# Performance work log

Hardware: AMD Instinct MI355X
Metric: run time of the kernel (lower is better)

The kernel has to match this reference:

```python
import jax, jax.numpy as jnp
import numpy as np

NUM_HEADS = 12
EPS = 1e-6


def setup_inputs() -> dict:
    key = jax.random.key(0)
    k1, k2, k3, k4 = jax.random.split(key, 4)
    N, B, D = 1025, 8, 768
    x = jax.random.normal(k1, (N, B, D), dtype=jnp.float32)
    # torch nn.Linear weights: [out_features, in_features]
    w_qkv = jax.random.normal(k2, (3 * D, D), dtype=jnp.float32) * (D ** -0.5)
    w_proj = jax.random.normal(k3, (D, D), dtype=jnp.float32) * (D ** -0.5)
    b_proj = jax.random.normal(k4, (D,), dtype=jnp.float32) * 0.01
    return {"x": x, "w_qkv": w_qkv, "w_proj": w_proj, "b_proj": b_proj}


def reference(x, w_qkv, w_proj, b_proj):
    N, B, D = x.shape
    H = NUM_HEADS
    hd = D // H
    scale = hd ** -0.5
    scale_vv = scale * 1.0  # scale_multiplier = 1.0

    xb = jnp.transpose(x, (1, 0, 2))  # [B, N, D]
    qkv = xb @ w_qkv.T  # [B, N, 3D]
    qkv = qkv.reshape(B, N, 3, H, hd).transpose(2, 0, 3, 1, 4)  # [3, B, H, N, hd]
    q, k, v = qkv[0], qkv[1], qkv[2]

    # QK path: only row 0 of out_ori survives the masking, compute just that row
    scores0 = jnp.einsum('bhqd,bhkd->bhqk', q[:, :, :1], k) * scale  # [B,H,1,N]
    attn0 = jax.nn.softmax(scores0, axis=-1)
    out0 = jnp.einsum('bhqk,bhkd->bhqd', attn0, v)  # [B,H,1,hd]

    # VV cosine path: only rows 1: survive
    vn = v / jnp.maximum(jnp.linalg.norm(v, axis=-1, keepdims=True), EPS)
    scores_vv = jnp.einsum('bhqd,bhkd->bhqk', vn[:, :, 1:], vn) * scale_vv  # [B,H,N-1,N]
    attn_vv = jax.nn.softmax(scores_vv, axis=-1)
    out_vv = jnp.einsum('bhqk,bhkd->bhqd', attn_vv, v)  # [B,H,N-1,hd]

    out = jnp.concatenate([out0, out_vv], axis=2)  # [B,H,N,hd]
    out = out.transpose(0, 2, 1, 3).reshape(B, N, D)
    out = out @ w_proj.T + b_proj
    return jnp.transpose(out, (1, 0, 2))  # [N, B, D]
```

## Files before the change

kernel.cpp:

```cpp
#include <hip/hip_runtime.h>

typedef unsigned short u16;
typedef unsigned int   u32;
typedef __attribute__((ext_vector_type(8))) short short8;
typedef __attribute__((ext_vector_type(4))) float f32x4;

#define AS1 __attribute__((address_space(1)))
#define AS3 __attribute__((address_space(3)))

#define NSEQ  1025
#define BB    8
#define DD    768
#define HH    12
#define MROWS 8200
#define MPAD  8320
#define KPAD  1088

__device__ __forceinline__ void gl2lds16(const void* g, void* l) {
  __builtin_amdgcn_global_load_lds((const AS1 u32*)g, (AS3 u32*)l, 16, 0, 0);
}
__device__ __forceinline__ u16 f2bf(float f) {
  u32 u = __float_as_uint(f);
  return (u16)((u + 0x7FFFu + ((u >> 16) & 1u)) >> 16);
}
__device__ __forceinline__ float bf2f(u16 u) { return __uint_as_float(((u32)u) << 16); }

__global__ __launch_bounds__(256) void prep(const float* __restrict__ x,
                                            const float* __restrict__ wqkv,
                                            const float* __restrict__ wproj,
                                            u16* __restrict__ xb,
                                            u16* __restrict__ wkv,
                                            u16* __restrict__ wpj) {
  const int XB_G  = MPAD * 192;
  const int WKV_G = 1536 * 192;
  const int WPJ_G = 768 * 192;
  int g = blockIdx.x * 256 + threadIdx.x;
  float4 v;
  u16* dst;
  size_t di;
  if (g < XB_G) {
    int m = g / 192, e4 = g - m * 192;
    if (m < MROWS) {
      int bb = m / NSEQ, ns = m - bb * NSEQ;
      v = ((const float4*)x)[(size_t)(ns * BB + bb) * 192 + e4];
    } else {
      v.x = v.y = v.z = v.w = 0.f;
    }
    dst = xb; di = (size_t)g;
  } else if (g < XB_G + WKV_G) {
    int r = g - XB_G;
    v = ((const float4*)wqkv)[(size_t)147456 + r];
    dst = wkv; di = (size_t)r;
  } else if (g < XB_G + WKV_G + WPJ_G) {
    int r = g - XB_G - WKV_G;
    v = ((const float4*)wproj)[r];
    dst = wpj; di = (size_t)r;
  } else {
    return;
  }
  uint2 o;
  o.x = (u32)f2bf(v.x) | ((u32)f2bf(v.y) << 16);
  o.y = (u32)f2bf(v.z) | ((u32)f2bf(v.w) << 16);
  ((uint2*)dst)[di] = o;
}

template <int MODE, int NT>
__global__ __launch_bounds__(256) void gemm_bt(const u16* __restrict__ A,
                                               const u16* __restrict__ W,
                                               u16* __restrict__ Cbf,
                                               float* __restrict__ Cf,
                                               const float* __restrict__ bias,
                                               int ldc) {
  __shared__ u16 sA[128 * 64];
  __shared__ u16 sW[128 * 64];
  const int id = blockIdx.x;
  const int rx = id & 7, qx = id >> 3;
  const int kq = qx / NT;
  const int m_t = rx + (kq << 3);
  if (m_t > 64) return;
  const int n_t = qx - kq * NT;
  const int m0 = m_t << 7, n0 = n_t << 7;

  const int tid = threadIdx.x;
  const int w = tid >> 6, lane = tid & 63;
  const int wm = w & 1, wn = w >> 1;
  const int lc = lane & 15, lr = lane >> 4;

  f32x4 zero4 = {0.f, 0.f, 0.f, 0.f};
  f32x4 acc[4][4];
#pragma unroll
  for (int i = 0; i < 4; ++i)
#pragma unroll
    for (int j = 0; j < 4; ++j) acc[i][j] = zero4;

  const int r0 = tid >> 3;
  const int ko = (tid & 7) << 3;
  const u16* gA = A + (size_t)(m0 + r0) * DD + ko;
  const u16* gW = W + (size_t)(n0 + r0) * DD + ko;
  char* lA = (char*)sA + tid * 16;
  char* lW = (char*)sW + tid * 16;

#pragma unroll 1
  for (int kt = 0; kt < 12; ++kt) {
    __syncthreads();
#pragma unroll
    for (int j = 0; j < 4; ++j) {
      gl2lds16(gA + (size_t)j * 32 * DD + kt * 64, lA + j * 4096);
      gl2lds16(gW + (size_t)j * 32 * DD + kt * 64, lW + j * 4096);
    }
    __syncthreads();
#pragma unroll
    for (int kk = 0; kk < 2; ++kk) {
      short8 af[4], wf[4];
#pragma unroll
      for (int mt = 0; mt < 4; ++mt)
        af[mt] = *(const short8*)((char*)sA + ((wm << 6) + (mt << 4) + lc) * 128 + (kk << 6) + (lr << 4));
#pragma unroll
      for (int nt = 0; nt < 4; ++nt)
        wf[nt] = *(const short8*)((char*)sW + ((wn << 6) + (nt << 4) + lc) * 128 + (kk << 6) + (lr << 4));
#pragma unroll
      for (int mt = 0; mt < 4; ++mt)
#pragma unroll
        for (int nt = 0; nt < 4; ++nt)
          acc[mt][nt] = __builtin_amdgcn_mfma_f32_16x16x32_bf16(af[mt], wf[nt], acc[mt][nt], 0, 0, 0);
    }
  }

  if (MODE == 0) {
#pragma unroll
    for (int mt = 0; mt < 4; ++mt)
#pragma unroll
      for (int r = 0; r < 4; ++r) {
        int m = m0 + (wm << 6) + (mt << 4) + (lr << 2) + r;
        if (m < MROWS) {
          size_t base = (size_t)m * ldc + n0 + (wn << 6) + lc;
#pragma unroll
          for (int nt = 0; nt < 4; ++nt) Cbf[base + (nt << 4)] = f2bf(acc[mt][nt][r]);
        }
      }
  } else {
    float b4[4];
#pragma unroll
    for (int nt = 0; nt < 4; ++nt) b4[nt] = bias[n0 + (wn << 6) + (nt << 4) + lc];
#pragma unroll
    for (int mt = 0; mt < 4; ++mt)
#pragma unroll
      for (int r = 0; r < 4; ++r) {
        int m = m0 + (wm << 6) + (mt << 4) + (lr << 2) + r;
        if (m < MROWS) {
          int bb = m / NSEQ;
          int ns = m - bb * NSEQ;
          float* o = Cf + (size_t)ns * (BB * DD) + bb * DD + n0 + (wn << 6) + lc;
#pragma unroll
          for (int nt = 0; nt < 4; ++nt) o[nt << 4] = acc[mt][nt][r] + b4[nt];
        }
      }
  }
}

__global__ __launch_bounds__(256) void q0_kernel(const float* __restrict__ x,
                                                 const float* __restrict__ wq,
                                                 float* __restrict__ q0) {
  __shared__ float red[256];
  int bid = blockIdx.x;
  int b = bid / HH, c = bid - b * HH;
  int tid = threadIdx.x;
  int dp = (c << 6) + (tid >> 2), part = tid & 3;
  const float4* x4 = (const float4*)(x + (size_t)b * DD + part * 192);
  const float4* w4 = (const float4*)(wq + (size_t)dp * DD + part * 192);
  float acc = 0.f;
#pragma unroll 4
  for (int e = 0; e < 48; ++e) {
    float4 a = x4[e], w = w4[e];
    acc += a.x * w.x + a.y * w.y + a.z * w.z + a.w * w.w;
  }
  red[tid] = acc;
  __syncthreads();
  if (part == 0) q0[b * DD + dp] = red[tid] + red[tid + 1] + red[tid + 2] + red[tid + 3];
}

__global__ __launch_bounds__(256) void transpose_v(const u16* __restrict__ kv,
                                                   u16* __restrict__ vT,
                                                   u16* __restrict__ vn) {
  __shared__ u16 tile[64][72];
  __shared__ float red[256];
  __shared__ float sInv[64];
  int bid = blockIdx.x;
  int kc = bid % 17;
  int t2 = bid / 17;
  int h = t2 % HH, b = t2 / HH;
  int tid = threadIdx.x;
  int kl = tid >> 2, dc = (tid & 3) << 4;
  int key = kc * 64 + kl;
  u32 vals[8];
  if (key < NSEQ) {
    const u32* g = (const u32*)(kv + ((size_t)b * NSEQ + key) * 1536 + DD + h * 64 + dc);
#pragma unroll
    for (int i = 0; i < 8; ++i) vals[i] = g[i];
  } else {
#pragma unroll
    for (int i = 0; i < 8; ++i) vals[i] = 0;
  }
  float part = 0.f;
#pragma unroll
  for (int i = 0; i < 8; ++i) {
    float a = bf2f((u16)(vals[i] & 0xFFFF));
    float c = bf2f((u16)(vals[i] >> 16));
    part += a * a + c * c;
    ((u32*)&tile[kl][dc])[i] = vals[i];
  }
  red[tid] = part;
  __syncthreads();
  if ((tid & 3) == 0) {
    float s = red[tid] + red[tid + 1] + red[tid + 2] + red[tid + 3];
    sInv[kl] = (key < NSEQ) ? 1.0f / fmaxf(sqrtf(s), 1e-6f) : 0.0f;
  }
  __syncthreads();
  float iv = sInv[kl];
  u32 ovn[8];
#pragma unroll
  for (int i = 0; i < 8; ++i) {
    float a = bf2f((u16)(vals[i] & 0xFFFF)) * iv;
    float c = bf2f((u16)(vals[i] >> 16)) * iv;
    ovn[i] = (u32)f2bf(a) | ((u32)f2bf(c) << 16);
  }
  u32* on = (u32*)(vn + ((size_t)(b * HH + h) * KPAD + key) * 64 + dc);
#pragma unroll
  for (int i = 0; i < 8; ++i) on[i] = ovn[i];
  int dl = tid >> 2, ks = (tid & 3) << 4;
  u32 ov[8];
#pragma unroll
  for (int i = 0; i < 8; ++i)
    ov[i] = (u32)tile[ks + 2 * i][dl] | ((u32)tile[ks + 2 * i + 1][dl] << 16);
  u16* o = vT + (size_t)(b * HH + h) * 64 * KPAD + (size_t)dl * KPAD + kc * 64 + ks;
#pragma unroll
  for (int i = 0; i < 8; ++i) ((u32*)o)[i] = ov[i];
}

__global__ __launch_bounds__(256) void row0_attn(const float* __restrict__ q0,
                                                 const u16* __restrict__ kv,
                                                 u16* __restrict__ attn) {
  __shared__ float sq[64];
  __shared__ float sc[NSEQ];
  __shared__ float red[256];
  __shared__ float rpv[32][68];
  int bid = blockIdx.x;
  int b = bid / HH, h = bid - b * HH;
  int tid = threadIdx.x;
  if (tid < 64) sq[tid] = q0[b * DD + h * 64 + tid];
  __syncthreads();
  float mx = -1e30f;
  for (int n = tid; n < NSEQ; n += 256) {
    const u32* kr = (const u32*)(kv + ((size_t)b * NSEQ + n) * 1536 + h * 64);
    float s = 0.f;
#pragma unroll
    for (int i = 0; i < 32; ++i) {
      u32 u = kr[i];
      s += bf2f((u16)(u & 0xFFFF)) * sq[2 * i] + bf2f((u16)(u >> 16)) * sq[2 * i + 1];
    }
    s *= 0.125f;
    sc[n] = s;
    mx = fmaxf(mx, s);
  }
  red[tid] = mx;
  __syncthreads();
  for (int st = 128; st > 0; st >>= 1) {
    if (tid < st) red[tid] = fmaxf(red[tid], red[tid + st]);
    __syncthreads();
  }
  mx = red[0];
  __syncthreads();
  float ds = 0.f;
  for (int n = tid; n < NSEQ; n += 256) {
    float p = __expf(sc[n] - mx);
    sc[n] = p;
    ds += p;
  }
  red[tid] = ds;
  __syncthreads();
  for (int st = 128; st > 0; st >>= 1) {
    if (tid < st) red[tid] += red[tid + st];
    __syncthreads();
  }
  float den = red[0];
  __syncthreads();

  int kp = tid >> 3, dc = (tid & 7) << 3;
  const u16* vb = kv + (size_t)b * NSEQ * 1536 + DD + h * 64 + dc;
  float acc[8];
#pragma unroll
  for (int i = 0; i < 8; ++i) acc[i] = 0.f;
#pragma unroll 4
  for (int j = 0; j < 32; ++j) {
    int n = kp + (j << 5);
    uint4 v = *(const uint4*)(vb + (size_t)n * 1536);
    float p = sc[n];
    acc[0] += p * bf2f((u16)(v.x & 0xFFFF));
    acc[1] += p * bf2f((u16)(v.x >> 16));
    acc[2] += p * bf2f((u16)(v.y & 0xFFFF));
    acc[3] += p * bf2f((u16)(v.y >> 16));
    acc[4] += p * bf2f((u16)(v.z & 0xFFFF));
    acc[5] += p * bf2f((u16)(v.z >> 16));
    acc[6] += p * bf2f((u16)(v.w & 0xFFFF));
    acc[7] += p * bf2f((u16)(v.w >> 16));
  }
  if (kp == 0) {
    uint4 v = *(const uint4*)(vb + (size_t)1024 * 1536);
    float p = sc[1024];
    acc[0] += p * bf2f((u16)(v.x & 0xFFFF));
    acc[1] += p * bf2f((u16)(v.x >> 16));
    acc[2] += p * bf2f((u16)(v.y & 0xFFFF));
    acc[3] += p * bf2f((u16)(v.y >> 16));
    acc[4] += p * bf2f((u16)(v.z & 0xFFFF));
    acc[5] += p * bf2f((u16)(v.z >> 16));
    acc[6] += p * bf2f((u16)(v.w & 0xFFFF));
    acc[7] += p * bf2f((u16)(v.w >> 16));
  }
#pragma unroll
  for (int i = 0; i < 8; ++i) rpv[kp][dc + i] = acc[i];
  __syncthreads();
  if (tid < 64) {
    float s = 0.f;
#pragma unroll
    for (int p = 0; p < 32; ++p) s += rpv[p][tid];
    attn[(size_t)b * NSEQ * DD + h * 64 + tid] = f2bf(s / den);
  }
}

__global__ __launch_bounds__(256, 4) void vv_attn(const u16* __restrict__ vn,
                                                  const u16* __restrict__ vT,
                                                  u16* __restrict__ attn) {
  __shared__ u16 sQ[2 * 8 * 64 * 8];
  __shared__ u16 sK[2 * 4 * 64 * 8];
  __shared__ u16 sV[2 * 4 * 64 * 8];
  __shared__ u16 sP[4 * 2 * 64 * 8];

  const int tid = threadIdx.x, w = tid >> 6, lane = tid & 63;
  const int lc = lane & 15, lr = lane >> 4;
  const int bh = blockIdx.x;
  const int m0 = blockIdx.y << 7;
  const int b = bh / HH, h = bh - b * HH;
  const char* nb = (const char*)(vn + (size_t)bh * KPAD * 64);
  const char* tb = (const char*)(vT + (size_t)bh * 64 * KPAD);

#pragma unroll
  for (int j = 0; j < 4; ++j) {
    int lin = (w << 12) + (j << 10) + (lane << 4);
    int kk = lin >> 13, qg = (lin >> 10) & 7;
    int lr2 = (lin >> 8) & 3, lc2 = (lin >> 4) & 15;
    gl2lds16(nb + (size_t)(1 + m0 + (qg << 4) + lc2) * 128 + (kk << 6) + (lr2 << 4),
             (char*)sQ + lin);
  }

  const char* srcK[2];
  const char* srcV[2];
  char* dstK[2];
  char* dstV[2];
#pragma unroll
  for (int j = 0; j < 2; ++j) {
    int lin = (w << 11) + (j << 10) + (lane << 4);
    int kk = lin >> 12, kg = (lin >> 10) & 3;
    int lr2 = (lin >> 8) & 3, lc2 = (lin >> 4) & 15;
    srcK[j] = nb + (size_t)((kg << 4) + lc2) * 128 + (kk << 6) + (lr2 << 4);
    srcV[j] = tb + (size_t)((kg << 4) + lc2) * (KPAD * 2) + (kk << 6) + (lr2 << 4);
    dstK[j] = (char*)sK + lin;
    dstV[j] = (char*)sV + lin;
  }

  f32x4 zero4 = {0.f, 0.f, 0.f, 0.f};
  f32x4 oacc[2][4];
  f32x4 dacc[2];
#pragma unroll
  for (int i = 0; i < 2; ++i) {
    dacc[i] = zero4;
#pragma unroll
    for (int j = 0; j < 4; ++j) oacc[i][j] = zero4;
  }
  short8 ones;
#pragma unroll
  for (int i = 0; i < 8; ++i) ones[i] = (short)0x3F80;

  const float CEXP = 0.1803368801111204f;

  const char* rdK = (const char*)sK + (lane << 4);
  const char* rdQ = (const char*)sQ + ((w << 1) << 10) + (lane << 4);
  const char* rdV = (const char*)sV + (lane << 4);
  const char* rdP = (const char*)sP + (w << 11) + (lane << 4);
  char* wrP = (char*)sP + (w << 11) + ((lr >> 1) << 8) + (lc << 4) + ((lr & 1) << 3);

#pragma unroll 1
  for (int kt = 0; kt < 17; ++kt) {
    __syncthreads();
#pragma unroll
    for (int j = 0; j < 2; ++j) {
      gl2lds16(srcK[j] + (size_t)kt * 8192, dstK[j]);
      gl2lds16(srcV[j] + (size_t)kt * 128, dstV[j]);
    }
    __syncthreads();

    f32x4 sacc[4][2];
#pragma unroll
    for (int mt = 0; mt < 4; ++mt)
#pragma unroll
      for (int nt = 0; nt < 2; ++nt) sacc[mt][nt] = zero4;
#pragma unroll
    for (int kk = 0; kk < 2; ++kk) {
      short8 ak[4], bq[2];
#pragma unroll
      for (int mt = 0; mt < 4; ++mt)
        ak[mt] = *(const short8*)(rdK + (kk << 12) + (mt << 10));
#pragma unroll
      for (int nt = 0; nt < 2; ++nt)
        bq[nt] = *(const short8*)(rdQ + (kk << 13) + (nt << 10));
#pragma unroll
      for (int mt = 0; mt < 4; ++mt)
#pragma unroll
        for (int nt = 0; nt < 2; ++nt)
          sacc[mt][nt] = __builtin_amdgcn_mfma_f32_16x16x32_bf16(ak[mt], bq[nt], sacc[mt][nt], 0, 0, 0);
    }

#pragma unroll
    for (int h2 = 0; h2 < 2; ++h2) {
      if (!(kt == 16 && h2 == 1)) {
        asm volatile("" ::: "memory");
#pragma unroll
        for (int mi = 0; mi < 2; ++mi) {
          int ms = (h2 << 1) + mi;
#pragma unroll
          for (int nt = 0; nt < 2; ++nt) {
            f32x4 s = sacc[ms][nt];
            u32 a0 = __float_as_uint(__builtin_amdgcn_exp2f(s[0] * CEXP)) + 0x8000u;
            u32 a1 = __float_as_uint(__builtin_amdgcn_exp2f(s[1] * CEXP)) + 0x8000u;
            u32 a2 = __float_as_uint(__builtin_amdgcn_exp2f(s[2] * CEXP)) + 0x8000u;
            u32 a3 = __float_as_uint(__builtin_amdgcn_exp2f(s[3] * CEXP)) + 0x8000u;
            uint2 pv;
            pv.x = __builtin_amdgcn_perm(a1, a0, 0x07060302u);
            pv.y = __builtin_amdgcn_perm(a3, a2, 0x07060302u);
            if (kt == 16) {
              pv.x = (ms == 0 && lr == 0) ? (pv.x & 0xFFFFu) : 0u;
              pv.y = 0u;
            }
            *(uint2*)(wrP + (nt << 10) + (mi << 9)) = pv;
          }
        }
        __builtin_amdgcn_sched_barrier(0);
        asm volatile("" ::: "memory");
        short8 ap[2], bv[4];
#pragma unroll
        for (int mt = 0; mt < 2; ++mt)
          ap[mt] = *(const short8*)(rdP + (mt << 10));
#pragma unroll
        for (int nt = 0; nt < 4; ++nt)
          bv[nt] = *(const short8*)(rdV + (h2 << 12) + (nt << 10));
#pragma unroll
        for (int mt = 0; mt < 2; ++mt) {
#pragma unroll
          for (int nt = 0; nt < 4; ++nt)
            oacc[mt][nt] = __builtin_amdgcn_mfma_f32_16x16x32_bf16(ap[mt], bv[nt], oacc[mt][nt], 0, 0, 0);
          dacc[mt] = __builtin_amdgcn_mfma_f32_16x16x32_bf16(ap[mt], ones, dacc[mt], 0, 0, 0);
        }
      }
    }
  }

#pragma unroll
  for (int mt = 0; mt < 2; ++mt) {
#pragma unroll
    for (int r = 0; r < 4; ++r) {
      int q = (w << 5) + (mt << 4) + (lr << 2) + r;
      int nseq = 1 + m0 + q;
      float rdn = 1.0f / dacc[mt][r];
      size_t obase = ((size_t)b * NSEQ + nseq) * DD + h * 64 + lc;
#pragma unroll
      for (int nt = 0; nt < 4; ++nt) attn[obase + (nt << 4)] = f2bf(oacc[mt][nt][r] * rdn);
    }
  }
}

extern "C" void kernel_launch(void* const* d_in, const int* in_sizes, int n_in,
                              void* d_out, int out_size, void* d_ws, size_t ws_size,
                              hipStream_t stream) {
  const float* x      = (const float*)d_in[0];
  const float* w_qkv  = (const float*)d_in[1];
  const float* w_proj = (const float*)d_in[2];
  const float* b_proj = (const float*)d_in[3];
  float* out = (float*)d_out;
  char* ws = (char*)d_ws;

  u16*   xb   = (u16*)(ws + 0);
  u16*   vT   = (u16*)(ws + 0);
  u16*   wkv  = (u16*)(ws + 13369344);
  u16*   wpj  = (u16*)(ws + 15728640);
  u16*   kvb  = (u16*)(ws + 16908288);
  float* q0   = (float*)(ws + 42467328);
  u16*   attn = (u16*)(ws + 42491904);
  u16*   vn   = (u16*)(ws + 55271424);

  prep<<<7968, 256, 0, stream>>>(x, w_qkv, w_proj, xb, wkv, wpj);
  gemm_bt<0, 12><<<864, 256, 0, stream>>>(xb, wkv, kvb, nullptr, nullptr, 1536);
  q0_kernel<<<96, 256, 0, stream>>>(x, w_qkv, q0);
  transpose_v<<<1632, 256, 0, stream>>>(kvb, vT, vn);
  row0_attn<<<96, 256, 0, stream>>>(q0, kvb, attn);
  vv_attn<<<dim3(96, 8), 256, 0, stream>>>(vn, vT, attn);
  gemm_bt<1, 6><<<432, 256, 0, stream>>>(attn, wpj, nullptr, out, b_proj, 768);
}
```

Before: 219.4 us.

## Double-buffer K/V tiles in vv_attn, keep Q in registers, fuse q0 into prep

The vv_attn loop now prefetches the next K/V tile into an alternate LDS buffer while computing the current one, removing one barrier per iteration. Q fragments are loaded once into registers instead of being staged in LDS. The separate q0 projection kernel is merged into the prep launch as extra blocks, saving a launch. These changes raise register and LDS use, and correctness depends on async LDS loads completing before the single barrier.

```diff
diff --git a/kernel.cpp b/kernel.cpp
--- a/kernel.cpp
+++ b/kernel.cpp
@@ -30,10 +30,30 @@
                                             const float* __restrict__ wproj,
                                             u16* __restrict__ xb,
                                             u16* __restrict__ wkv,
-                                            u16* __restrict__ wpj) {
+                                            u16* __restrict__ wpj,
+                                            float* __restrict__ q0) {
+  __shared__ float red[256];
   const int XB_G  = MPAD * 192;
   const int WKV_G = 1536 * 192;
   const int WPJ_G = 768 * 192;
+  if (blockIdx.x >= 7968) {
+    int bid = blockIdx.x - 7968;
+    int b = bid / HH, c = bid - b * HH;
+    int tid = threadIdx.x;
+    int dp = (c << 6) + (tid >> 2), part = tid & 3;
+    const float4* x4 = (const float4*)(x + (size_t)b * DD + part * 192);
+    const float4* w4 = (const float4*)(wqkv + (size_t)dp * DD + part * 192);
+    float acc = 0.f;
+#pragma unroll 4
+    for (int e = 0; e < 48; ++e) {
+      float4 a = x4[e], w = w4[e];
+      acc += a.x * w.x + a.y * w.y + a.z * w.z + a.w * w.w;
+    }
+    red[tid] = acc;
+    __syncthreads();
+    if (part == 0) q0[b * DD + dp] = red[tid] + red[tid + 1] + red[tid + 2] + red[tid + 3];
+    return;
+  }
   int g = blockIdx.x * 256 + threadIdx.x;
   float4 v;
   u16* dst;
@@ -158,27 +178,6 @@
   }
 }
 
-__global__ __launch_bounds__(256) void q0_kernel(const float* __restrict__ x,
-                                                 const float* __restrict__ wq,
-                                                 float* __restrict__ q0) {
-  __shared__ float red[256];
-  int bid = blockIdx.x;
-  int b = bid / HH, c = bid - b * HH;
-  int tid = threadIdx.x;
-  int dp = (c << 6) + (tid >> 2), part = tid & 3;
-  const float4* x4 = (const float4*)(x + (size_t)b * DD + part * 192);
-  const float4* w4 = (const float4*)(wq + (size_t)dp * DD + part * 192);
-  float acc = 0.f;
-#pragma unroll 4
-  for (int e = 0; e < 48; ++e) {
-    float4 a = x4[e], w = w4[e];
-    acc += a.x * w.x + a.y * w.y + a.z * w.z + a.w * w.w;
-  }
-  red[tid] = acc;
-  __syncthreads();
-  if (part == 0) q0[b * DD + dp] = red[tid] + red[tid + 1] + red[tid + 2] + red[tid + 3];
-}
-
 __global__ __launch_bounds__(256) void transpose_v(const u16* __restrict__ kv,
                                                    u16* __restrict__ vT,
                                                    u16* __restrict__ vn) {
@@ -330,10 +329,9 @@
 __global__ __launch_bounds__(256, 4) void vv_attn(const u16* __restrict__ vn,
                                                   const u16* __restrict__ vT,
                                                   u16* __restrict__ attn) {
-  __shared__ u16 sQ[2 * 8 * 64 * 8];
-  __shared__ u16 sK[2 * 4 * 64 * 8];
-  __shared__ u16 sV[2 * 4 * 64 * 8];
-  __shared__ u16 sP[4 * 2 * 64 * 8];
+  __shared__ u16 sK[2][4096];
+  __shared__ u16 sV[2][4096];
+  __shared__ u16 sP[4096];
 
   const int tid = threadIdx.x, w = tid >> 6, lane = tid & 63;
   const int lc = lane & 15, lr = lane >> 4;
@@ -343,19 +341,17 @@
   const char* nb = (const char*)(vn + (size_t)bh * KPAD * 64);
   const char* tb = (const char*)(vT + (size_t)bh * 64 * KPAD);
 
-#pragma unroll
-  for (int j = 0; j < 4; ++j) {
-    int lin = (w << 12) + (j << 10) + (lane << 4);
-    int kk = lin >> 13, qg = (lin >> 10) & 7;
-    int lr2 = (lin >> 8) & 3, lc2 = (lin >> 4) & 15;
-    gl2lds16(nb + (size_t)(1 + m0 + (qg << 4) + lc2) * 128 + (kk << 6) + (lr2 << 4),
-             (char*)sQ + lin);
-  }
+  short8 qreg[2][2];
+#pragma unroll
+  for (int kk = 0; kk < 2; ++kk)
+#pragma unroll
+    for (int nt = 0; nt < 2; ++nt)
+      qreg[kk][nt] = *(const short8*)(nb +
+          (size_t)(1 + m0 + (w << 5) + (nt << 4) + lc) * 128 + (kk << 6) + (lr << 4));
 
   const char* srcK[2];
   const char* srcV[2];
-  char* dstK[2];
-  char* dstV[2];
+  int offKV[2];
 #pragma unroll
   for (int j = 0; j < 2; ++j) {
     int lin = (w << 11) + (j << 10) + (lane << 4);
@@ -363,8 +359,7 @@
     int lr2 = (lin >> 8) & 3, lc2 = (lin >> 4) & 15;
     srcK[j] = nb + (size_t)((kg << 4) + lc2) * 128 + (kk << 6) + (lr2 << 4);
     srcV[j] = tb + (size_t)((kg << 4) + lc2) * (KPAD * 2) + (kk << 6) + (lr2 << 4);
-    dstK[j] = (char*)sK + lin;
-    dstV[j] = (char*)sV + lin;
+    offKV[j] = lin;
   }
 
   f32x4 zero4 = {0.f, 0.f, 0.f, 0.f};
@@ -382,21 +377,28 @@
 
   const float CEXP = 0.1803368801111204f;
 
-  const char* rdK = (const char*)sK + (lane << 4);
-  const char* rdQ = (const char*)sQ + ((w << 1) << 10) + (lane << 4);
-  const char* rdV = (const char*)sV + (lane << 4);
   const char* rdP = (const char*)sP + (w << 11) + (lane << 4);
   char* wrP = (char*)sP + (w << 11) + ((lr >> 1) << 8) + (lc << 4) + ((lr & 1) << 3);
 
+#pragma unroll
+  for (int j = 0; j < 2; ++j) {
+    gl2lds16(srcK[j], (char*)sK + offKV[j]);
+    gl2lds16(srcV[j], (char*)sV + offKV[j]);
+  }
+
 #pragma unroll 1
   for (int kt = 0; kt < 17; ++kt) {
+    const int cur = kt & 1;
     __syncthreads();
-#pragma unroll
-    for (int j = 0; j < 2; ++j) {
-      gl2lds16(srcK[j] + (size_t)kt * 8192, dstK[j]);
-      gl2lds16(srcV[j] + (size_t)kt * 128, dstV[j]);
-    }
-    __syncthreads();
+    if (kt < 16) {
+#pragma unroll
+      for (int j = 0; j < 2; ++j) {
+        gl2lds16(srcK[j] + (size_t)(kt + 1) * 8192, (char*)sK + (cur ^ 1) * 8192 + offKV[j]);
+        gl2lds16(srcV[j] + (size_t)(kt + 1) * 128,  (char*)sV + (cur ^ 1) * 8192 + offKV[j]);
+      }
+    }
+    const char* rdK = (const char*)sK + cur * 8192 + (lane << 4);
+    const char* rdV = (const char*)sV + cur * 8192 + (lane << 4);
 
     f32x4 sacc[4][2];
 #pragma unroll
@@ -405,18 +407,15 @@
       for (int nt = 0; nt < 2; ++nt) sacc[mt][nt] = zero4;
 #pragma unroll
     for (int kk = 0; kk < 2; ++kk) {
-      short8 ak[4], bq[2];
+      short8 ak[4];
 #pragma unroll
       for (int mt = 0; mt < 4; ++mt)
         ak[mt] = *(const short8*)(rdK + (kk << 12) + (mt << 10));
 #pragma unroll
-      for (int nt = 0; nt < 2; ++nt)
-        bq[nt] = *(const short8*)(rdQ + (kk << 13) + (nt << 10));
-#pragma unroll
       for (int mt = 0; mt < 4; ++mt)
 #pragma unroll
         for (int nt = 0; nt < 2; ++nt)
-          sacc[mt][nt] = __builtin_amdgcn_mfma_f32_16x16x32_bf16(ak[mt], bq[nt], sacc[mt][nt], 0, 0, 0);
+          sacc[mt][nt] = __builtin_amdgcn_mfma_f32_16x16x32_bf16(ak[mt], qreg[kk][nt], sacc[mt][nt], 0, 0, 0);
     }
 
 #pragma unroll
@@ -496,9 +495,8 @@
   u16*   attn = (u16*)(ws + 42491904);
   u16*   vn   = (u16*)(ws + 55271424);
 
-  prep<<<7968, 256, 0, stream>>>(x, w_qkv, w_proj, xb, wkv, wpj);
+  prep<<<8064, 256, 0, stream>>>(x, w_qkv, w_proj, xb, wkv, wpj, q0);
   gemm_bt<0, 12><<<864, 256, 0, stream>>>(xb, wkv, kvb, nullptr, nullptr, 1536);
-  q0_kernel<<<96, 256, 0, stream>>>(x, w_qkv, q0);
   transpose_v<<<1632, 256, 0, stream>>>(kvb, vT, vn);
   row0_attn<<<96, 256, 0, stream>>>(q0, kvb, attn);
   vv_attn<<<dim3(96, 8), 256, 0, stream>>>(vn, vT, attn);
```

New measurement: 235.7 us. 1.07x slower.

## Halve vv_attn query tile to 64 rows and keep Q in registers

Applied to the files above, without the earlier changes.

The VV attention kernel now covers 64 query rows per block instead of 128, doubling the grid to 96x16 blocks. The Q tile is loaded straight into registers instead of staged in shared memory, and launch bounds are raised to 6 blocks per CU. Smaller LDS use and fewer accumulators are meant to raise occupancy and fill the 256 CUs better. In exchange, each K/V tile is reused across half as many queries, so K/V global and LDS traffic doubles.

```diff
diff --git a/kernel.cpp b/kernel.cpp
--- a/kernel.cpp
+++ b/kernel.cpp
@@ -327,35 +327,30 @@
   }
 }
 
-__global__ __launch_bounds__(256, 4) void vv_attn(const u16* __restrict__ vn,
+__global__ __launch_bounds__(256, 6) void vv_attn(const u16* __restrict__ vn,
                                                   const u16* __restrict__ vT,
                                                   u16* __restrict__ attn) {
-  __shared__ u16 sQ[2 * 8 * 64 * 8];
-  __shared__ u16 sK[2 * 4 * 64 * 8];
-  __shared__ u16 sV[2 * 4 * 64 * 8];
-  __shared__ u16 sP[4 * 2 * 64 * 8];
+  __shared__ u16 sK[4096];
+  __shared__ u16 sV[4096];
+  __shared__ u16 sP[2048];
 
   const int tid = threadIdx.x, w = tid >> 6, lane = tid & 63;
   const int lc = lane & 15, lr = lane >> 4;
   const int bh = blockIdx.x;
-  const int m0 = blockIdx.y << 7;
+  const int m0 = blockIdx.y << 6;
   const int b = bh / HH, h = bh - b * HH;
   const char* nb = (const char*)(vn + (size_t)bh * KPAD * 64);
   const char* tb = (const char*)(vT + (size_t)bh * 64 * KPAD);
 
-#pragma unroll
-  for (int j = 0; j < 4; ++j) {
-    int lin = (w << 12) + (j << 10) + (lane << 4);
-    int kk = lin >> 13, qg = (lin >> 10) & 7;
-    int lr2 = (lin >> 8) & 3, lc2 = (lin >> 4) & 15;
-    gl2lds16(nb + (size_t)(1 + m0 + (qg << 4) + lc2) * 128 + (kk << 6) + (lr2 << 4),
-             (char*)sQ + lin);
-  }
+  short8 qreg[2];
+#pragma unroll
+  for (int kk = 0; kk < 2; ++kk)
+    qreg[kk] = *(const short8*)(nb +
+        (size_t)(1 + m0 + (w << 4) + lc) * 128 + (kk << 6) + (lr << 4));
 
   const char* srcK[2];
   const char* srcV[2];
-  char* dstK[2];
-  char* dstV[2];
+  int offKV[2];
 #pragma unroll
   for (int j = 0; j < 2; ++j) {
     int lin = (w << 11) + (j << 10) + (lane << 4);
@@ -363,19 +358,14 @@
     int lr2 = (lin >> 8) & 3, lc2 = (lin >> 4) & 15;
     srcK[j] = nb + (size_t)((kg << 4) + lc2) * 128 + (kk << 6) + (lr2 << 4);
     srcV[j] = tb + (size_t)((kg << 4) + lc2) * (KPAD * 2) + (kk << 6) + (lr2 << 4);
-    dstK[j] = (char*)sK + lin;
-    dstV[j] = (char*)sV + lin;
+    offKV[j] = lin;
   }
 
   f32x4 zero4 = {0.f, 0.f, 0.f, 0.f};
-  f32x4 oacc[2][4];
-  f32x4 dacc[2];
-#pragma unroll
-  for (int i = 0; i < 2; ++i) {
-    dacc[i] = zero4;
-#pragma unroll
-    for (int j = 0; j < 4; ++j) oacc[i][j] = zero4;
-  }
+  f32x4 oacc[4];
+  f32x4 dacc = zero4;
+#pragma unroll
+  for (int j = 0; j < 4; ++j) oacc[j] = zero4;
   short8 ones;
 #pragma unroll
   for (int i = 0; i < 8; ++i) ones[i] = (short)0x3F80;
@@ -383,40 +373,32 @@
   const float CEXP = 0.1803368801111204f;
 
   const char* rdK = (const char*)sK + (lane << 4);
-  const char* rdQ = (const char*)sQ + ((w << 1) << 10) + (lane << 4);
   const char* rdV = (const char*)sV + (lane << 4);
-  const char* rdP = (const char*)sP + (w << 11) + (lane << 4);
-  char* wrP = (char*)sP + (w << 11) + ((lr >> 1) << 8) + (lc << 4) + ((lr & 1) << 3);
+  const char* rdP = (const char*)sP + (w << 10) + (lane << 4);
+  char* wrP = (char*)sP + (w << 10) + ((lr >> 1) << 8) + (lc << 4) + ((lr & 1) << 3);
 
 #pragma unroll 1
   for (int kt = 0; kt < 17; ++kt) {
     __syncthreads();
 #pragma unroll
     for (int j = 0; j < 2; ++j) {
-      gl2lds16(srcK[j] + (size_t)kt * 8192, dstK[j]);
-      gl2lds16(srcV[j] + (size_t)kt * 128, dstV[j]);
-    }
-    __syncthreads();
-
-    f32x4 sacc[4][2];
-#pragma unroll
-    for (int mt = 0; mt < 4; ++mt)
-#pragma unroll
-      for (int nt = 0; nt < 2; ++nt) sacc[mt][nt] = zero4;
+      gl2lds16(srcK[j] + (size_t)kt * 8192, (char*)sK + offKV[j]);
+      gl2lds16(srcV[j] + (size_t)kt * 128,  (char*)sV + offKV[j]);
+    }
+    __syncthreads();
+
+    f32x4 sacc[4];
+#pragma unroll
+    for (int mt = 0; mt < 4; ++mt) sacc[mt] = zero4;
 #pragma unroll
     for (int kk = 0; kk < 2; ++kk) {
-      short8 ak[4], bq[2];
+      short8 ak[4];
 #pragma unroll
       for (int mt = 0; mt < 4; ++mt)
         ak[mt] = *(const short8*)(rdK + (kk << 12) + (mt << 10));
 #pragma unroll
-      for (int nt = 0; nt < 2; ++nt)
-        bq[nt] = *(const short8*)(rdQ + (kk << 13) + (nt << 10));
-#pragma unroll
       for (int mt = 0; mt < 4; ++mt)
-#pragma unroll
-        for (int nt = 0; nt < 2; ++nt)
-          sacc[mt][nt] = __builtin_amdgcn_mfma_f32_16x16x32_bf16(ak[mt], bq[nt], sacc[mt][nt], 0, 0, 0);
+        sacc[mt] = __builtin_amdgcn_mfma_f32_16x16x32_bf16(ak[mt], qreg[kk], sacc[mt], 0, 0, 0);
     }
 
 #pragma unroll
@@ -426,54 +408,43 @@
 #pragma unroll
         for (int mi = 0; mi < 2; ++mi) {
           int ms = (h2 << 1) + mi;
-#pragma unroll
-          for (int nt = 0; nt < 2; ++nt) {
-            f32x4 s = sacc[ms][nt];
-            u32 a0 = __float_as_uint(__builtin_amdgcn_exp2f(s[0] * CEXP)) + 0x8000u;
-            u32 a1 = __float_as_uint(__builtin_amdgcn_exp2f(s[1] * CEXP)) + 0x8000u;
-            u32 a2 = __float_as_uint(__builtin_amdgcn_exp2f(s[2] * CEXP)) + 0x8000u;
-            u32 a3 = __float_as_uint(__builtin_amdgcn_exp2f(s[3] * CEXP)) + 0x8000u;
-            uint2 pv;
-            pv.x = __builtin_amdgcn_perm(a1, a0, 0x07060302u);
-            pv.y = __builtin_amdgcn_perm(a3, a2, 0x07060302u);
-            if (kt == 16) {
-              pv.x = (ms == 0 && lr == 0) ? (pv.x & 0xFFFFu) : 0u;
-              pv.y = 0u;
-            }
-            *(uint2*)(wrP + (nt << 10) + (mi << 9)) = pv;
+          f32x4 s = sacc[ms];
+          u32 a0 = __float_as_uint(__builtin_amdgcn_exp2f(s[0] * CEXP)) + 0x8000u;
+          u32 a1 = __float_as_uint(__builtin_amdgcn_exp2f(s[1] * CEXP)) + 0x8000u;
+          u32 a2 = __float_as_uint(__builtin_amdgcn_exp2f(s[2] * CEXP)) + 0x8000u;
+          u32 a3 = __float_as_uint(__builtin_amdgcn_exp2f(s[3] * CEXP)) + 0x8000u;
+          uint2 pv;
+          pv.x = __builtin_amdgcn_perm(a1, a0, 0x07060302u);
+          pv.y = __builtin_amdgcn_perm(a3, a2, 0x07060302u);
+          if (kt == 16) {
+            pv.x = (mi == 0 && lr == 0) ? (pv.x & 0xFFFFu) : 0u;
+            pv.y = 0u;
           }
+          *(uint2*)(wrP + (mi << 9)) = pv;
         }
         __builtin_amdgcn_sched_barrier(0);
         asm volatile("" ::: "memory");
-        short8 ap[2], bv[4];
-#pragma unroll
-        for (int mt = 0; mt < 2; ++mt)
-          ap[mt] = *(const short8*)(rdP + (mt << 10));
+        short8 ap = *(const short8*)rdP;
+        short8 bv[4];
 #pragma unroll
         for (int nt = 0; nt < 4; ++nt)
           bv[nt] = *(const short8*)(rdV + (h2 << 12) + (nt << 10));
 #pragma unroll
-        for (int mt = 0; mt < 2; ++mt) {
-#pragma unroll
-          for (int nt = 0; nt < 4; ++nt)
-            oacc[mt][nt] = __builtin_amdgcn_mfma_f32_16x16x32_bf16(ap[mt], bv[nt], oacc[mt][nt], 0, 0, 0);
-          dacc[mt] = __builtin_amdgcn_mfma_f32_16x16x32_bf16(ap[mt], ones, dacc[mt], 0, 0, 0);
-        }
+        for (int nt = 0; nt < 4; ++nt)
+          oacc[nt] = __builtin_amdgcn_mfma_f32_16x16x32_bf16(ap, bv[nt], oacc[nt], 0, 0, 0);
+        dacc = __builtin_amdgcn_mfma_f32_16x16x32_bf16(ap, ones, dacc, 0, 0, 0);
       }
     }
   }
 
 #pragma unroll
-  for (int mt = 0; mt < 2; ++mt) {
-#pragma unroll
-    for (int r = 0; r < 4; ++r) {
-      int q = (w << 5) + (mt << 4) + (lr << 2) + r;
-      int nseq = 1 + m0 + q;
-      float rdn = 1.0f / dacc[mt][r];
-      size_t obase = ((size_t)b * NSEQ + nseq) * DD + h * 64 + lc;
-#pragma unroll
-      for (int nt = 0; nt < 4; ++nt) attn[obase + (nt << 4)] = f2bf(oacc[mt][nt][r] * rdn);
-    }
+  for (int r = 0; r < 4; ++r) {
+    int q = (w << 4) + (lr << 2) + r;
+    int nseq = 1 + m0 + q;
+    float rdn = 1.0f / dacc[r];
+    size_t obase = ((size_t)b * NSEQ + nseq) * DD + h * 64 + lc;
+#pragma unroll
+    for (int nt = 0; nt < 4; ++nt) attn[obase + (nt << 4)] = f2bf(oacc[nt][r] * rdn);
   }
 }
 
@@ -501,6 +472,6 @@
   q0_kernel<<<96, 256, 0, stream>>>(x, w_qkv, q0);
   transpose_v<<<1632, 256, 0, stream>>>(kvb, vT, vn);
   row0_attn<<<96, 256, 0, stream>>>(q0, kvb, attn);
-  vv_attn<<<dim3(96, 8), 256, 0, stream>>>(vn, vT, attn);
+  vv_attn<<<dim3(96, 16), 256, 0, stream>>>(vn, vT, attn);
   gemm_bt<1, 6><<<432, 256, 0, stream>>>(attn, wpj, nullptr, out, b_proj, 768);
 }
```

After: 236.0 us. +7.6%, slower.
